# Performance work log

Measured on AMD Instinct MI355X. Metric: run time of the kernel, lower is better.

Reference implementation:

```python
import jax, jax.numpy as jnp
import numpy as np

N = 50000        # nodes
DEG = 32         # in-degree per node
E = N * DEG      # edges
T = 4            # towers
NODE = 128       # node_dim
OUT = 128        # out_dim
IN_T = NODE // T   # 32, divide_input tower slice
OUT_T = OUT // T   # 32
AVG_D_LOG = float(np.log(5.0))  # avg_d = {'log': log(4+1)}
EPS = 1e-5


def setup_inputs() -> dict:
    key = jax.random.key(0)
    ks = jax.random.split(key, 6)
    h = jax.random.normal(ks[0], (N, NODE), jnp.float32)
    src = jax.random.randint(ks[1], (E,), 0, N)
    # every node gets exactly DEG incoming edges (sorted dst)
    dst = jnp.repeat(jnp.arange(N), DEG)
    # per-tower pretrans MLP (1 layer): Linear(2*IN_T -> OUT_T)
    W_pre = jax.random.normal(ks[2], (T, 2 * IN_T, OUT_T), jnp.float32) * 0.05
    b_pre = jnp.zeros((T, OUT_T), jnp.float32)
    # per-tower posttrans MLP (1 layer): Linear(12*OUT_T + IN_T -> OUT_T)
    W_post = jax.random.normal(ks[3], (T, 12 * OUT_T + IN_T, OUT_T), jnp.float32) * 0.05
    b_post = jnp.zeros((T, OUT_T), jnp.float32)
    # mixing network: Linear(OUT -> OUT) + LeakyReLU
    W_mix = jax.random.normal(ks[4], (OUT, OUT), jnp.float32) * 0.05
    b_mix = jnp.zeros((OUT,), jnp.float32)
    return dict(h=h, src=src, dst=dst, W_pre=W_pre, b_pre=b_pre,
                W_post=W_post, b_post=b_post, W_mix=W_mix, b_mix=b_mix)


def _pna_forward(h, src, dst, W_pre, b_pre, W_post, b_post, W_mix, b_mix):
    ht = h.reshape(N, T, IN_T)                    # divide_input: tower slices
    z2 = jnp.concatenate([ht[src], ht[dst]], axis=-1)   # [E,T,2*IN_T] (src||dst)
    # pretrans: MLP(1 layer) then ReLU
    e = jax.nn.relu(jnp.einsum('etk,tko->eto', z2, W_pre) + b_pre)  # [E,T,OUT_T]

    deg = jax.ops.segment_sum(jnp.ones((E,), h.dtype), dst, num_segments=N)  # [N]
    deg_c = jnp.maximum(deg, 1.0)[:, None, None]
    seg = lambda x: jax.ops.segment_sum(x, dst, num_segments=N)
    mean = seg(e) / deg_c                          # [N,T,OUT_T]
    mean_sq = seg(e * e) / deg_c
    std = jnp.sqrt(jax.nn.relu(mean_sq - mean * mean) + EPS)
    mx = jax.ops.segment_max(e, dst, num_segments=N)
    mn = jax.ops.segment_min(e, dst, num_segments=N)
    agg = jnp.concatenate([mean, mx, mn, std], axis=-1)   # [N,T,4*OUT_T]

    # scalers: identity, amplification, attenuation (D = in-degree)
    sc = jnp.log(deg + 1.0) / AVG_D_LOG            # [N]
    amp = agg * sc[:, None, None]
    att = agg / jnp.maximum(sc, EPS)[:, None, None]
    h_agg = jnp.concatenate([agg, amp, att], axis=-1)     # [N,T,12*OUT_T]

    # posttrans: cat(h_tower, aggregated) -> MLP(1 layer) -> ReLU
    z = jnp.concatenate([ht, h_agg], axis=-1)      # [N,T,IN_T+12*OUT_T]
    hp = jax.nn.relu(jnp.einsum('ntk,tko->nto', z, W_post) + b_post)  # [N,T,OUT_T]
    h_cat = hp.reshape(N, OUT)

    h_out = jax.nn.leaky_relu(h_cat @ W_mix + b_mix, 0.01)
    return h + h_out                               # residual (node_dim == out_dim)


def reference(h, src, dst, W_pre, b_pre, W_post, b_post, W_mix, b_mix):
    return _pna_forward(h, src, dst, W_pre, b_pre, W_post, b_post, W_mix, b_mix)
```

## Files before the change

kernel.cpp:

```cpp
#include <hip/hip_runtime.h>
#include <hip/hip_bf16.h>
#include <hip/hip_fp16.h>
#include <math.h>

#define N_NODES 50000
#define DEG     32
#define NBF     16
#define EPSV    1e-5f

typedef __attribute__((ext_vector_type(8))) short short8;
typedef __attribute__((ext_vector_type(4))) float f32x4;
typedef __attribute__((ext_vector_type(2))) _Float16 h16x2;
typedef __attribute__((ext_vector_type(4))) unsigned int uint4v;

__device__ __forceinline__ unsigned int bfpack(float a, float b) {
    return (unsigned int)__bfloat16_as_ushort(__float2bfloat16(a)) |
           ((unsigned int)__bfloat16_as_ushort(__float2bfloat16(b)) << 16);
}

__global__ __launch_bounds__(256) void k_proj(const float* __restrict__ h,
        const float* __restrict__ W_pre, const float* __restrict__ b_pre,
        const float* __restrict__ W_post, const float* __restrict__ W_mix,
        __hip_bfloat16* __restrict__ WeffT, __hip_bfloat16* __restrict__ WmixT,
        _Float16* __restrict__ Pd, _Float16* __restrict__ Ps, float sc, float isc) {
    int tid = threadIdx.x, w = tid >> 6, lane = tid & 63;
    int nb = blockIdx.x * 64;

    if (blockIdx.x < 144) {
        int i = blockIdx.x * 256 + tid;
        if (i < 20480) {
            int k = i % 160, to = i / 160, o = to & 31, t = to >> 5;
            const float* Wt = W_post + t * 416 * 32;
            float v;
            if (k < 32) v = Wt[k * 32 + o];
            else {
                int g = k - 32;
                v = Wt[(32 + g) * 32 + o] + sc * Wt[(160 + g) * 32 + o]
                  + isc * Wt[(288 + g) * 32 + o];
            }
            WeffT[i] = __float2bfloat16(v);
        } else {
            int j = i - 20480;
            int k = j & 127, o = j >> 7;
            WmixT[j] = __float2bfloat16(W_mix[k * 128 + o]);
        }
    }

    __shared__ __align__(16) __hip_bfloat16 sA[64][136];
    __shared__ __align__(16) _Float16 sP[2][64][136];
    int colc = (tid & 31) * 4, rowb = tid >> 5;
#pragma unroll
    for (int i = 0; i < 8; ++i) {
        int row = i * 8 + rowb, n = nb + row;
        unsigned int lo = 0, hi = 0;
        if (n < N_NODES) {
            float4 f = *(const float4*)(h + n * 128 + colc);
            lo = bfpack(f.x, f.y); hi = bfpack(f.z, f.w);
        }
        *(uint2*)(&sA[row][colc]) = make_uint2(lo, hi);
    }
    __syncthreads();
    int col = lane & 15, quad = lane >> 4, r0 = w * 16;
    short8 a[4];
#pragma unroll
    for (int t = 0; t < 4; ++t)
        a[t] = *(const short8*)(&sA[r0 + col][t * 32 + quad * 8]);

#pragma unroll
    for (int half = 0; half < 2; ++half) {
#pragma unroll
        for (int t = 0; t < 4; ++t) {
#pragma unroll
            for (int ct = 0; ct < 2; ++ct) {
                int o = ct * 16 + col;
                const float* wp = W_pre + t * 2048 + (half * 32 + quad * 8) * 32 + o;
                unsigned int bw0 = bfpack(wp[0],   wp[32]);
                unsigned int bw1 = bfpack(wp[64],  wp[96]);
                unsigned int bw2 = bfpack(wp[128], wp[160]);
                unsigned int bw3 = bfpack(wp[192], wp[224]);
                uint4v bwv = {bw0, bw1, bw2, bw3};
                short8 b = __builtin_bit_cast(short8, bwv);
                f32x4 acc = {0.f, 0.f, 0.f, 0.f};
                acc = __builtin_amdgcn_mfma_f32_16x16x32_bf16(a[t], b, acc, 0, 0, 0);
                float bp = half ? b_pre[t * 32 + o] : 0.f;
#pragma unroll
                for (int r = 0; r < 4; ++r)
                    sP[half][r0 + quad * 4 + r][t * 32 + o] =
                        __float2half(acc[r] + bp);
            }
        }
    }
    __syncthreads();

#pragma unroll
    for (int half = 0; half < 2; ++half) {
        _Float16* dst = half ? Pd : Ps;
#pragma unroll
        for (int rr = 0; rr < 4; ++rr) {
            int chunk = rr * 256 + tid;
            int row = chunk >> 4, seg = chunk & 15, n = nb + row;
            if (n < N_NODES)
                *(uint4v*)(dst + n * 128 + seg * 8) =
                    *(const uint4v*)(&sP[half][row][seg * 8]);
        }
    }
}

__global__ __launch_bounds__(256) void k_fused(const float* __restrict__ h,
        const int* __restrict__ src, const _Float16* __restrict__ Pd,
        const _Float16* __restrict__ Ps, const __hip_bfloat16* __restrict__ WeffT,
        const __hip_bfloat16* __restrict__ WmixT, const float* __restrict__ b_post,
        const float* __restrict__ b_mix, float* __restrict__ out) {
    __shared__ __align__(16) __hip_bfloat16 sZ[NBF][648];
    __shared__ __align__(16) __hip_bfloat16 sHp[NBF][136];
    int tid = threadIdx.x, w = tid >> 6, lane = tid & 63;
    int nb = blockIdx.x * NBF;

    int lid = lane & 31, hsel = lane & 32;
    int cq = lid * 4;
    int tA = cq >> 5, oA = cq & 31;
    const h16x2 zeroh = {(_Float16)0.f, (_Float16)0.f};
    const h16x2 bigh  = {(_Float16)65504.f, (_Float16)65504.f};
#pragma unroll
    for (int it = 0; it < 2; ++it) {
        int row = it * 8 + w + (hsel >> 3);
        int n = nb + row;
        int vsrc = src[n * DEG + lid];
        float4 hv = *(const float4*)(h + n * 128 + cq);
        uint2 pdu = *(const uint2*)(Pd + n * 128 + cq);
        h16x2 pd01 = __builtin_bit_cast(h16x2, pdu.x);
        h16x2 pd23 = __builtin_bit_cast(h16x2, pdu.y);
        h16x2 sum01 = zeroh, sum23 = zeroh, sq01 = zeroh, sq23 = zeroh;
        h16x2 mx01 = zeroh, mx23 = zeroh;
        h16x2 mn01 = bigh, mn23 = bigh;
#pragma unroll
        for (int j0 = 0; j0 < DEG; j0 += 16) {
            uint2 pv[16];
#pragma unroll
            for (int u = 0; u < 16; ++u) {
                int s = __shfl(vsrc, (j0 + u) | hsel);
                pv[u] = *(const uint2*)(Ps + s * 128 + cq);
            }
#pragma unroll
            for (int u = 0; u < 16; ++u) {
                h16x2 f01 = __builtin_bit_cast(h16x2, pv[u].x);
                h16x2 f23 = __builtin_bit_cast(h16x2, pv[u].y);
                h16x2 e01 = __builtin_elementwise_max(f01 + pd01, zeroh);
                h16x2 e23 = __builtin_elementwise_max(f23 + pd23, zeroh);
                sum01 += e01; sq01 = e01 * e01 + sq01;
                mx01 = __builtin_elementwise_max(mx01, e01);
                mn01 = __builtin_elementwise_min(mn01, e01);
                sum23 += e23; sq23 = e23 * e23 + sq23;
                mx23 = __builtin_elementwise_max(mx23, e23);
                mn23 = __builtin_elementwise_min(mn23, e23);
            }
        }
        float mean0 = (float)sum01.x * (1.f / DEG), mean1 = (float)sum01.y * (1.f / DEG);
        float mean2 = (float)sum23.x * (1.f / DEG), mean3 = (float)sum23.y * (1.f / DEG);
        float sd0 = sqrtf(fmaxf((float)sq01.x * (1.f / DEG) - mean0 * mean0, 0.f) + EPSV);
        float sd1 = sqrtf(fmaxf((float)sq01.y * (1.f / DEG) - mean1 * mean1, 0.f) + EPSV);
        float sd2 = sqrtf(fmaxf((float)sq23.x * (1.f / DEG) - mean2 * mean2, 0.f) + EPSV);
        float sd3 = sqrtf(fmaxf((float)sq23.y * (1.f / DEG) - mean3 * mean3, 0.f) + EPSV);
        unsigned int* zr = (unsigned int*)(&sZ[row][tA * 160 + oA]);
        zr[0]  = bfpack(hv.x, hv.y);               zr[1]  = bfpack(hv.z, hv.w);
        zr[16] = bfpack(mean0, mean1);             zr[17] = bfpack(mean2, mean3);
        zr[32] = bfpack((float)mx01.x, (float)mx01.y);
        zr[33] = bfpack((float)mx23.x, (float)mx23.y);
        zr[48] = bfpack((float)mn01.x, (float)mn01.y);
        zr[49] = bfpack((float)mn23.x, (float)mn23.y);
        zr[64] = bfpack(sd0, sd1);                 zr[65] = bfpack(sd2, sd3);
    }
    __syncthreads();

    int col = lane & 15, quad = lane >> 4;
#pragma unroll
    for (int i = 0; i < 2; ++i) {
        int ct = w * 2 + i, t = ct >> 1, nt = ct & 1;
        f32x4 acc = {0.f, 0.f, 0.f, 0.f};
        int oc = t * 32 + nt * 16 + col;
        const __hip_bfloat16* wrow = WeffT + oc * 160 + quad * 8;
#pragma unroll
        for (int ks = 0; ks < 5; ++ks) {
            short8 a = *(const short8*)(&sZ[col][t * 160 + ks * 32 + quad * 8]);
            short8 b = *(const short8*)(wrow + ks * 32);
            acc = __builtin_amdgcn_mfma_f32_16x16x32_bf16(a, b, acc, 0, 0, 0);
        }
        float bp = b_post[oc];
#pragma unroll
        for (int r = 0; r < 4; ++r)
            sHp[quad * 4 + r][oc] = __float2bfloat16(fmaxf(acc[r] + bp, 0.f));
    }
    __syncthreads();

#pragma unroll
    for (int i = 0; i < 2; ++i) {
        int nt = w * 2 + i;
        f32x4 acc = {0.f, 0.f, 0.f, 0.f};
        int oc = nt * 16 + col;
        const __hip_bfloat16* wrow = WmixT + oc * 128 + quad * 8;
#pragma unroll
        for (int ks = 0; ks < 4; ++ks) {
            short8 a = *(const short8*)(&sHp[col][ks * 32 + quad * 8]);
            short8 b = *(const short8*)(wrow + ks * 32);
            acc = __builtin_amdgcn_mfma_f32_16x16x32_bf16(a, b, acc, 0, 0, 0);
        }
        float bm = b_mix[oc];
#pragma unroll
        for (int r = 0; r < 4; ++r) {
            int n = nb + quad * 4 + r;
            float m = acc[r] + bm;
            m = m > 0.f ? m : 0.01f * m;
            out[n * 128 + oc] = h[n * 128 + oc] + m;
        }
    }
}

extern "C" void kernel_launch(void* const* d_in, const int* in_sizes, int n_in,
                              void* d_out, int out_size, void* d_ws, size_t ws_size,
                              hipStream_t stream) {
    const float* h      = (const float*)d_in[0];
    const int*   src    = (const int*)d_in[1];
    const float* W_pre  = (const float*)d_in[3];
    const float* b_pre  = (const float*)d_in[4];
    const float* W_post = (const float*)d_in[5];
    const float* b_post = (const float*)d_in[6];
    const float* W_mix  = (const float*)d_in[7];
    const float* b_mix  = (const float*)d_in[8];
    float* out = (float*)d_out;

    char* ws = (char*)d_ws;
    __hip_bfloat16* WeffT = (__hip_bfloat16*)ws;
    __hip_bfloat16* WmixT = (__hip_bfloat16*)(ws + 40960);
    _Float16*       Pd    = (_Float16*)(ws + 81920);
    _Float16*       Ps    = (_Float16*)(ws + 81920 + 12800000);

    double scd = log(33.0) / log(5.0);
    float sc = (float)scd, isc = (float)(1.0 / scd);

    hipLaunchKernelGGL(k_proj, dim3((N_NODES + 63) / 64), dim3(256), 0, stream,
                       h, W_pre, b_pre, W_post, W_mix, WeffT, WmixT, Pd, Ps, sc, isc);
    hipLaunchKernelGGL(k_fused, dim3(N_NODES / NBF), dim3(256), 0, stream,
                       h, src, Pd, Ps, WeffT, WmixT, b_post, b_mix, out);
}
```

Before: 167.7 us.

## Split gather into tower-major per-tower kernel with intermediate buffer for matmul

```diff
diff --git a/kernel.cpp b/kernel.cpp
--- a/kernel.cpp
+++ b/kernel.cpp
@@ -6,6 +6,8 @@
 #define N_NODES 50000
 #define DEG     32
 #define NBF     16
+#define NBLK    3125
+#define TSZ     (N_NODES * 32)
 #define EPSV    1e-5f
 
 typedef __attribute__((ext_vector_type(8))) short short8;
@@ -22,7 +24,7 @@
         const float* __restrict__ W_pre, const float* __restrict__ b_pre,
         const float* __restrict__ W_post, const float* __restrict__ W_mix,
         __hip_bfloat16* __restrict__ WeffT, __hip_bfloat16* __restrict__ WmixT,
-        _Float16* __restrict__ Pd, _Float16* __restrict__ Ps, float sc, float isc) {
+        _Float16* __restrict__ PdT, _Float16* __restrict__ PsT, float sc, float isc) {
     int tid = threadIdx.x, w = tid >> 6, lane = tid & 63;
     int nb = blockIdx.x * 64;
 
@@ -94,21 +96,69 @@
 
 #pragma unroll
     for (int half = 0; half < 2; ++half) {
-        _Float16* dst = half ? Pd : Ps;
+        _Float16* dst = half ? PdT : PsT;
 #pragma unroll
         for (int rr = 0; rr < 4; ++rr) {
             int chunk = rr * 256 + tid;
             int row = chunk >> 4, seg = chunk & 15, n = nb + row;
+            int t = seg >> 2, s4 = seg & 3;
             if (n < N_NODES)
-                *(uint4v*)(dst + n * 128 + seg * 8) =
+                *(uint4v*)(dst + t * TSZ + n * 32 + s4 * 8) =
                     *(const uint4v*)(&sP[half][row][seg * 8]);
         }
     }
 }
 
-__global__ __launch_bounds__(256) void k_fused(const float* __restrict__ h,
-        const int* __restrict__ src, const _Float16* __restrict__ Pd,
-        const _Float16* __restrict__ Ps, const __hip_bfloat16* __restrict__ WeffT,
+__global__ __launch_bounds__(256) void k_gather(const int* __restrict__ src,
+        const _Float16* __restrict__ PsT, const _Float16* __restrict__ PdT,
+        unsigned int* __restrict__ zG) {
+    int tid = threadIdx.x, w = tid >> 6, lane = tid & 63;
+    int bx = blockIdx.x;
+    int t = bx / NBLK, nb = (bx - t * NBLK) * 16;
+    int qw = lane >> 4, lq = lane & 15;
+    int row = w * 4 + qw, n = nb + row;
+    int cq2 = lq * 2;
+    const _Float16* base = PsT + t * TSZ;
+
+    int vsrc0 = src[n * DEG + lq];
+    int vsrc1 = src[n * DEG + 16 + lq];
+    unsigned int pdu = *(const unsigned int*)(PdT + t * TSZ + n * 32 + cq2);
+    h16x2 pd = __builtin_bit_cast(h16x2, pdu);
+
+    const h16x2 zeroh = {(_Float16)0.f, (_Float16)0.f};
+    const h16x2 bigh  = {(_Float16)65504.f, (_Float16)65504.f};
+    h16x2 sum = zeroh, sq = zeroh, mx = zeroh, mn = bigh;
+
+#pragma unroll
+    for (int j0 = 0; j0 < DEG; j0 += 16) {
+        unsigned int pv[16];
+#pragma unroll
+        for (int u2 = 0; u2 < 16; ++u2) {
+            int u = j0 + u2;
+            int s = __shfl(u < 16 ? vsrc0 : vsrc1, (lane & 48) | (u & 15));
+            pv[u2] = *(const unsigned int*)(base + s * 32 + cq2);
+        }
+#pragma unroll
+        for (int u2 = 0; u2 < 16; ++u2) {
+            h16x2 f = __builtin_bit_cast(h16x2, pv[u2]);
+            h16x2 e = __builtin_elementwise_max(f + pd, zeroh);
+            sum += e; sq = e * e + sq;
+            mx = __builtin_elementwise_max(mx, e);
+            mn = __builtin_elementwise_min(mn, e);
+        }
+    }
+    float mean0 = (float)sum.x * (1.f / DEG), mean1 = (float)sum.y * (1.f / DEG);
+    float sd0 = sqrtf(fmaxf((float)sq.x * (1.f / DEG) - mean0 * mean0, 0.f) + EPSV);
+    float sd1 = sqrtf(fmaxf((float)sq.y * (1.f / DEG) - mean1 * mean1, 0.f) + EPSV);
+    unsigned int* zr = zG + ((size_t)n * 4 + t) * 64;
+    zr[lq]      = bfpack(mean0, mean1);
+    zr[16 + lq] = bfpack((float)mx.x, (float)mx.y);
+    zr[32 + lq] = bfpack((float)mn.x, (float)mn.y);
+    zr[48 + lq] = bfpack(sd0, sd1);
+}
+
+__global__ __launch_bounds__(256) void k_mm(const float* __restrict__ h,
+        const unsigned int* __restrict__ zG, const __hip_bfloat16* __restrict__ WeffT,
         const __hip_bfloat16* __restrict__ WmixT, const float* __restrict__ b_post,
         const float* __restrict__ b_mix, float* __restrict__ out) {
     __shared__ __align__(16) __hip_bfloat16 sZ[NBF][648];
@@ -116,59 +166,22 @@
     int tid = threadIdx.x, w = tid >> 6, lane = tid & 63;
     int nb = blockIdx.x * NBF;
 
-    int lid = lane & 31, hsel = lane & 32;
-    int cq = lid * 4;
-    int tA = cq >> 5, oA = cq & 31;
-    const h16x2 zeroh = {(_Float16)0.f, (_Float16)0.f};
-    const h16x2 bigh  = {(_Float16)65504.f, (_Float16)65504.f};
-#pragma unroll
-    for (int it = 0; it < 2; ++it) {
-        int row = it * 8 + w + (hsel >> 3);
-        int n = nb + row;
-        int vsrc = src[n * DEG + lid];
-        float4 hv = *(const float4*)(h + n * 128 + cq);
-        uint2 pdu = *(const uint2*)(Pd + n * 128 + cq);
-        h16x2 pd01 = __builtin_bit_cast(h16x2, pdu.x);
-        h16x2 pd23 = __builtin_bit_cast(h16x2, pdu.y);
-        h16x2 sum01 = zeroh, sum23 = zeroh, sq01 = zeroh, sq23 = zeroh;
-        h16x2 mx01 = zeroh, mx23 = zeroh;
-        h16x2 mn01 = bigh, mn23 = bigh;
-#pragma unroll
-        for (int j0 = 0; j0 < DEG; j0 += 16) {
-            uint2 pv[16];
-#pragma unroll
-            for (int u = 0; u < 16; ++u) {
-                int s = __shfl(vsrc, (j0 + u) | hsel);
-                pv[u] = *(const uint2*)(Ps + s * 128 + cq);
-            }
-#pragma unroll
-            for (int u = 0; u < 16; ++u) {
-                h16x2 f01 = __builtin_bit_cast(h16x2, pv[u].x);
-                h16x2 f23 = __builtin_bit_cast(h16x2, pv[u].y);
-                h16x2 e01 = __builtin_elementwise_max(f01 + pd01, zeroh);
-                h16x2 e23 = __builtin_elementwise_max(f23 + pd23, zeroh);
-                sum01 += e01; sq01 = e01 * e01 + sq01;
-                mx01 = __builtin_elementwise_max(mx01, e01);
-                mn01 = __builtin_elementwise_min(mn01, e01);
-                sum23 += e23; sq23 = e23 * e23 + sq23;
-                mx23 = __builtin_elementwise_max(mx23, e23);
-                mn23 = __builtin_elementwise_min(mn23, e23);
-            }
-        }
-        float mean0 = (float)sum01.x * (1.f / DEG), mean1 = (float)sum01.y * (1.f / DEG);
-        float mean2 = (float)sum23.x * (1.f / DEG), mean3 = (float)sum23.y * (1.f / DEG);
-        float sd0 = sqrtf(fmaxf((float)sq01.x * (1.f / DEG) - mean0 * mean0, 0.f) + EPSV);
-        float sd1 = sqrtf(fmaxf((float)sq01.y * (1.f / DEG) - mean1 * mean1, 0.f) + EPSV);
-        float sd2 = sqrtf(fmaxf((float)sq23.x * (1.f / DEG) - mean2 * mean2, 0.f) + EPSV);
-        float sd3 = sqrtf(fmaxf((float)sq23.y * (1.f / DEG) - mean3 * mean3, 0.f) + EPSV);
-        unsigned int* zr = (unsigned int*)(&sZ[row][tA * 160 + oA]);
-        zr[0]  = bfpack(hv.x, hv.y);               zr[1]  = bfpack(hv.z, hv.w);
-        zr[16] = bfpack(mean0, mean1);             zr[17] = bfpack(mean2, mean3);
-        zr[32] = bfpack((float)mx01.x, (float)mx01.y);
-        zr[33] = bfpack((float)mx23.x, (float)mx23.y);
-        zr[48] = bfpack((float)mn01.x, (float)mn01.y);
-        zr[49] = bfpack((float)mn23.x, (float)mn23.y);
-        zr[64] = bfpack(sd0, sd1);                 zr[65] = bfpack(sd2, sd3);
+    {
+        int r = tid >> 4, j = tid & 15, n = nb + r;
+        unsigned int* zrow = (unsigned int*)(&sZ[r][0]);
+        int t = j >> 2, o8 = (j & 3) * 8;
+        const float* hp = h + n * 128 + t * 32 + o8;
+        float4 f0 = *(const float4*)(hp);
+        float4 f1 = *(const float4*)(hp + 4);
+        int ho = t * 80 + (o8 >> 1);
+        zrow[ho + 0] = bfpack(f0.x, f0.y);  zrow[ho + 1] = bfpack(f0.z, f0.w);
+        zrow[ho + 2] = bfpack(f1.x, f1.y);  zrow[ho + 3] = bfpack(f1.z, f1.w);
+        const unsigned int* zg = zG + (size_t)n * 256;
+#pragma unroll
+        for (int k = 0; k < 16; ++k) {
+            int tt = k >> 2, st = k & 3;
+            zrow[tt * 80 + 16 + st * 16 + j] = zg[tt * 64 + st * 16 + j];
+        }
     }
     __syncthreads();
 
@@ -231,14 +244,17 @@
     char* ws = (char*)d_ws;
     __hip_bfloat16* WeffT = (__hip_bfloat16*)ws;
     __hip_bfloat16* WmixT = (__hip_bfloat16*)(ws + 40960);
-    _Float16*       Pd    = (_Float16*)(ws + 81920);
-    _Float16*       Ps    = (_Float16*)(ws + 81920 + 12800000);
+    _Float16*       PsT   = (_Float16*)(ws + 81920);
+    _Float16*       PdT   = (_Float16*)(ws + 81920 + 12800000);
+    unsigned int*   zG    = (unsigned int*)(ws + 81920 + 25600000);
 
     double scd = log(33.0) / log(5.0);
     float sc = (float)scd, isc = (float)(1.0 / scd);
 
     hipLaunchKernelGGL(k_proj, dim3((N_NODES + 63) / 64), dim3(256), 0, stream,
-                       h, W_pre, b_pre, W_post, W_mix, WeffT, WmixT, Pd, Ps, sc, isc);
-    hipLaunchKernelGGL(k_fused, dim3(N_NODES / NBF), dim3(256), 0, stream,
-                       h, src, Pd, Ps, WeffT, WmixT, b_post, b_mix, out);
-}
+                       h, W_pre, b_pre, W_post, W_mix, WeffT, WmixT, PdT, PsT, sc, isc);
+    hipLaunchKernelGGL(k_gather, dim3(NBLK * 4), dim3(256), 0, stream,
+                       src, PsT, PdT, zG);
+    hipLaunchKernelGGL(k_mm, dim3(NBLK), dim3(256), 0, stream,
+                       h, zG, WeffT, WmixT, b_post, b_mix, out);
+}
```

Measured after the change: 179.2 us. +6.9%, slower.
